# Optimization experiments

Measured on AMD Instinct MI355X. Metric: run time of the kernel, lower is better.

Reference implementation:

```python
import jax, jax.numpy as jnp
import numpy as np

SD = 4          # spixel_downsize
EPS = 1e-5      # BatchNorm eps
SLOPE = 0.01    # nn.LeakyReLU() default negative_slope


def deconv3d(x, w, stride, pad):
    # w is in torch ConvTranspose3d layout: (in_ch, out_ch, kd, kh, kw).
    # Transposed conv == conv with lhs_dilation=stride, flipped kernel,
    # padding (k-1-p) per spatial dim.
    kd, kh, kw = w.shape[2], w.shape[3], w.shape[4]
    wc = jnp.transpose(jnp.flip(w, axis=(2, 3, 4)), (1, 0, 2, 3, 4))  # OIDHW
    pads = [(kd - 1 - pad[0],) * 2, (kh - 1 - pad[1],) * 2, (kw - 1 - pad[2],) * 2]
    return jax.lax.conv_general_dilated(
        x, wc, window_strides=(1, 1, 1), padding=pads,
        lhs_dilation=(stride, stride, stride),
        dimension_numbers=('NCDHW', 'OIDHW', 'NCDHW'))


def bn_lrelu(x, g, b, relu=True):
    # inference BatchNorm3d with running_mean=0, running_var=1 (fresh BN)
    scale = (g / jnp.sqrt(1.0 + EPS)).reshape(1, -1, 1, 1, 1)
    y = x * scale + b.reshape(1, -1, 1, 1, 1)
    return jax.nn.leaky_relu(y, SLOPE) if relu else y


def _sl(s):
    # shift s in {+1, 0, -1} -> (agg slice, cost slice) along one spatial dim
    if s == 1:
        return slice(SD, None), slice(None, -SD)
    if s == 0:
        return slice(None), slice(None)
    return slice(None, -SD), slice(SD, None)


def setup_inputs() -> dict:
    key = jax.random.key(0)
    ks = jax.random.split(key, 8)
    b, d, h, w = 1, 24, 64, 128
    f32 = jnp.float32
    cv1 = jax.random.normal(ks[0], (b, 32, d, h, w), f32)                 # cv[-1]
    cv0 = jax.random.normal(ks[1], (b, 16, 2 * d, 2 * h, 2 * w), f32)     # cv[-2]
    sp = jax.random.uniform(ks[2], (b, 9, 4 * h, 4 * w), f32)             # superpixel probs
    w0a = jax.random.normal(ks[3], (32, 32, 3, 1, 1), f32) * 0.05
    w0b = jax.random.normal(ks[4], (32, 16, 4, 2, 2), f32) * 0.05
    w1a = jax.random.normal(ks[5], (32, 16, 3, 1, 1), f32) * 0.05
    w1b = jax.random.normal(ks[6], (16, 1, 4, 2, 2), f32) * 0.05
    g0, g1, g2, g3 = (jnp.ones((c,), f32) for c in (32, 16, 16, 1))
    b0, b1, b2, b3 = (jnp.zeros((c,), f32) for c in (32, 16, 16, 1))
    return dict(cv1=cv1, cv0=cv0, sp=sp, w0a=w0a, w0b=w0b, w1a=w1a, w1b=w1b,
                g0=g0, g1=g1, g2=g2, g3=g3, b0=b0, b1=b1, b2=b2, b3=b3)


def reference(cv1, cv0, sp, w0a, w0b, w1a, w1b, g0, g1, g2, g3, b0, b1, b2, b3):
    # conv[0]: BasicConv(32->32, k(3,1,1), s1, p(1,0,0)) + BasicConv(32->16, k(4,2,2), s2, p(1,0,0))
    x = bn_lrelu(deconv3d(cv1, w0a, 1, (1, 0, 0)), g0, b0)
    x = bn_lrelu(deconv3d(x, w0b, 2, (1, 0, 0)), g1, b1)
    x = jnp.concatenate((x, cv0), axis=1)
    # conv[1] (sp==2 branch): 32->16 then 16->out_dim, bn=relu=bnrelu=True
    x = bn_lrelu(deconv3d(x, w1a, 1, (1, 0, 0)), g2, b2)
    cost = bn_lrelu(deconv3d(x, w1b, 2, (1, 0, 0)), g3, b3)  # (b, 1, 4d, 4h, 4w)

    sp5 = sp[:, None]  # (b, 1, 9, H, W)
    agg = jnp.zeros_like(cost)
    k = 0
    for hy in (1, 0, -1):        # 9 fixed superpixel-neighbor shifts
        ah, ch = _sl(hy)
        for wx in (1, 0, -1):
            aw, cw = _sl(wx)
            wgt = sp5[:, :, k, ah, aw][:, :, None]  # (b,1,1,H',W')
            agg = agg.at[:, :, :, ah, aw].add(cost[:, :, :, ch, cw] * wgt)
            k += 1
    return agg
```

## Files before the change

### kernel.cpp

```cpp
#include <hip/hip_runtime.h>
#include <hip/hip_bf16.h>

typedef __hip_bfloat16 bf16;

constexpr int cD0 = 24,  cH0 = 64,  cW0 = 128;
constexpr int cD1 = 48,  cH1 = 128, cW1 = 256;
constexpr int cD2 = 96,  cH2 = 256, cW2 = 512;
constexpr size_t PL0 = (size_t)cD0 * cH0 * cW0;
constexpr size_t PL1 = (size_t)cD1 * cH1 * cW1;
constexpr size_t PL2 = (size_t)cD2 * cH2 * cW2;

__device__ __forceinline__ float b2f(bf16 v) { return __bfloat162float(v); }
__device__ __forceinline__ bf16  f2b(float v) { return __float2bfloat16(v); }
__device__ __forceinline__ float lrelu(float v) { return v >= 0.f ? v : 0.01f * v; }
__device__ __forceinline__ float us2f(ushort u) { return __uint_as_float(((uint)u) << 16); }
__device__ __forceinline__ ushort f2us(float v) { return __bfloat16_as_ushort(f2b(v)); }

__global__ __launch_bounds__(256) void kA(const float* __restrict__ cv1,
                                          const float* __restrict__ w0a,
                                          const float* __restrict__ g0,
                                          const float* __restrict__ b0,
                                          bf16* __restrict__ x1) {
    __shared__ float lw[3][32][32];
    __shared__ float lsc[32], lbi[32];
    const int tid = threadIdx.x;
    for (int i = tid; i < 32 * 32 * 3; i += 256) {
        int ci = i / 96, r = i - ci * 96, co = r / 3, u = r - co * 3;
        lw[u][ci][co] = w0a[i];
    }
    if (tid < 32) {
        lsc[tid] = g0[tid] * (1.0f / sqrtf(1.0f + 1e-5f));
        lbi[tid] = b0[tid];
    }
    __syncthreads();

    const int pos = blockIdx.x * 256 + tid;
    const int x = pos & (cW0 - 1);
    const int y = (pos >> 7) & (cH0 - 1);
    const int z = pos >> 13;

    float acc[32];
    #pragma unroll
    for (int co = 0; co < 32; ++co) acc[co] = 0.f;

    #pragma unroll
    for (int u = 0; u < 3; ++u) {
        const int zi = z + 1 - u;
        if (zi < 0 || zi >= cD0) continue;
        const float* src = cv1 + (size_t)(zi * cH0 + y) * cW0 + x;
        float v[32];
        #pragma unroll
        for (int ci = 0; ci < 32; ++ci) v[ci] = src[ci * PL0];
        #pragma unroll
        for (int ci = 0; ci < 32; ++ci) {
            const float4* wp = (const float4*)&lw[u][ci][0];
            #pragma unroll
            for (int q = 0; q < 8; ++q) {
                float4 wv = wp[q];
                acc[4*q+0] += v[ci] * wv.x; acc[4*q+1] += v[ci] * wv.y;
                acc[4*q+2] += v[ci] * wv.z; acc[4*q+3] += v[ci] * wv.w;
            }
        }
    }
    #pragma unroll
    for (int co = 0; co < 32; ++co)
        x1[co * PL0 + (size_t)(z * cH0 + y) * cW0 + x] =
            f2b(lrelu(acc[co] * lsc[co] + lbi[co]));
}

__global__ __launch_bounds__(256) void kB(const bf16* __restrict__ x1,
                                          const float* __restrict__ w0b,
                                          const float* __restrict__ g1,
                                          const float* __restrict__ b1,
                                          bf16* __restrict__ x2) {
    __shared__ float lw[4][2][32][2][16];
    __shared__ float lsc[16], lbi[16];
    const int tid = threadIdx.x;
    for (int i = tid; i < 8192; i += 256) {
        int ci = i >> 8, co = (i >> 4) & 15, kd = (i >> 2) & 3, kh = (i >> 1) & 1, kw = i & 1;
        lw[kd][kh][ci][kw][co] = w0b[i];
    }
    if (tid < 16) {
        lsc[tid] = g1[tid] * (1.0f / sqrtf(1.0f + 1e-5f));
        lbi[tid] = b1[tid];
    }
    __syncthreads();

    const int t    = blockIdx.x * 256 + tid;
    const int lane = t & 63;
    const int wv_  = (t >> 6) & 3;
    const int b_   = t >> 8;
    const int oh = b_ & 127;
    const int od = (b_ >> 7) * 4 + wv_;
    const int ih = oh >> 1, kh = oh & 1;
    const int p  = (od + 1) & 1;
    const int iw0 = 2 * lane;

    float acc[4][16];
    #pragma unroll
    for (int k = 0; k < 4; ++k)
        #pragma unroll
        for (int co = 0; co < 16; ++co) acc[k][co] = 0.f;

    #pragma unroll
    for (int j = 0; j < 2; ++j) {
        const int kd = p + 2 * j;
        const int id = (od + 1 - kd) >> 1;
        if (id < 0 || id >= cD0) continue;
        const bf16* src = x1 + (size_t)(id * cH0 + ih) * cW0 + iw0;
        uint px[32];
        #pragma unroll
        for (int ci = 0; ci < 32; ++ci)
            px[ci] = *(const uint*)(src + ci * PL0);
        #pragma unroll
        for (int ci = 0; ci < 32; ++ci) {
            const float v0 = us2f((ushort)(px[ci] & 0xffffu));
            const float v1 = us2f((ushort)(px[ci] >> 16));
            const float4* wp0 = (const float4*)&lw[kd][kh][ci][0][0];
            const float4* wp1 = (const float4*)&lw[kd][kh][ci][1][0];
            #pragma unroll
            for (int q = 0; q < 4; ++q) {
                float4 w0 = wp0[q], w1 = wp1[q];
                acc[0][4*q+0] += v0 * w0.x; acc[0][4*q+1] += v0 * w0.y;
                acc[0][4*q+2] += v0 * w0.z; acc[0][4*q+3] += v0 * w0.w;
                acc[1][4*q+0] += v0 * w1.x; acc[1][4*q+1] += v0 * w1.y;
                acc[1][4*q+2] += v0 * w1.z; acc[1][4*q+3] += v0 * w1.w;
                acc[2][4*q+0] += v1 * w0.x; acc[2][4*q+1] += v1 * w0.y;
                acc[2][4*q+2] += v1 * w0.z; acc[2][4*q+3] += v1 * w0.w;
                acc[3][4*q+0] += v1 * w1.x; acc[3][4*q+1] += v1 * w1.y;
                acc[3][4*q+2] += v1 * w1.z; acc[3][4*q+3] += v1 * w1.w;
            }
        }
    }
    const size_t obase = (size_t)(od * cH1 + oh) * cW1 + 4 * lane;
    #pragma unroll
    for (int co = 0; co < 16; ++co) {
        ushort4 s;
        s.x = f2us(lrelu(acc[0][co] * lsc[co] + lbi[co]));
        s.y = f2us(lrelu(acc[1][co] * lsc[co] + lbi[co]));
        s.z = f2us(lrelu(acc[2][co] * lsc[co] + lbi[co]));
        s.w = f2us(lrelu(acc[3][co] * lsc[co] + lbi[co]));
        *(ushort4*)(x2 + co * PL1 + obase) = s;
    }
}

__global__ __launch_bounds__(256) void kD(const bf16* __restrict__ x2,
                                          const float* __restrict__ cv0,
                                          const float* __restrict__ w1a,
                                          const float* __restrict__ g2,
                                          const float* __restrict__ b2v,
                                          bf16* __restrict__ x3) {
    __shared__ float lw[3][32][16];
    __shared__ float lsc[16], lbi[16];
    const int tid = threadIdx.x;
    for (int i = tid; i < 1536; i += 256) {
        int ci = i / 48, r = i - ci * 48, co = r / 3, u = r - co * 3;
        lw[u][ci][co] = w1a[i];
    }
    if (tid < 16) {
        lsc[tid] = g2[tid] * (1.0f / sqrtf(1.0f + 1e-5f));
        lbi[tid] = b2v[tid];
    }
    __syncthreads();

    const int bid = blockIdx.x;
    const int b_  = (bid & 7) * 384 + (bid >> 3);
    const int zq = b_ % 12;
    const int yh = b_ / 12;
    const int h  = yh & 1;
    const int y  = yh >> 1;
    const int lane = tid & 63;
    const int wv_  = tid >> 6;
    const int z  = zq * 4 + wv_;
    const int x0 = h * 128 + 2 * lane;

    float acc[2][16];
    #pragma unroll
    for (int k = 0; k < 2; ++k)
        #pragma unroll
        for (int co = 0; co < 16; ++co) acc[k][co] = 0.f;

    #pragma unroll
    for (int u = 0; u < 3; ++u) {
        const int zi = z + 1 - u;
        if (zi < 0 || zi >= cD1) continue;
        const size_t base = (size_t)(zi * cH1 + y) * cW1 + x0;
        uint   px[16];
        float2 pc[16];
        #pragma unroll
        for (int ci = 0; ci < 16; ++ci)
            px[ci] = *(const uint*)(x2 + ci * PL1 + base);
        #pragma unroll
        for (int ci = 0; ci < 16; ++ci)
            pc[ci] = *(const float2*)(cv0 + ci * PL1 + base);
        #pragma unroll
        for (int ci = 0; ci < 16; ++ci) {
            const float v0 = us2f((ushort)(px[ci] & 0xffffu));
            const float v1 = us2f((ushort)(px[ci] >> 16));
            const float4* wp = (const float4*)&lw[u][ci][0];
            #pragma unroll
            for (int q = 0; q < 4; ++q) {
                float4 wv = wp[q];
                acc[0][4*q+0] += v0 * wv.x; acc[0][4*q+1] += v0 * wv.y;
                acc[0][4*q+2] += v0 * wv.z; acc[0][4*q+3] += v0 * wv.w;
                acc[1][4*q+0] += v1 * wv.x; acc[1][4*q+1] += v1 * wv.y;
                acc[1][4*q+2] += v1 * wv.z; acc[1][4*q+3] += v1 * wv.w;
            }
        }
        #pragma unroll
        for (int ci = 0; ci < 16; ++ci) {
            const float v0 = pc[ci].x, v1 = pc[ci].y;
            const float4* wp = (const float4*)&lw[u][16 + ci][0];
            #pragma unroll
            for (int q = 0; q < 4; ++q) {
                float4 wv = wp[q];
                acc[0][4*q+0] += v0 * wv.x; acc[0][4*q+1] += v0 * wv.y;
                acc[0][4*q+2] += v0 * wv.z; acc[0][4*q+3] += v0 * wv.w;
                acc[1][4*q+0] += v1 * wv.x; acc[1][4*q+1] += v1 * wv.y;
                acc[1][4*q+2] += v1 * wv.z; acc[1][4*q+3] += v1 * wv.w;
            }
        }
    }
    const size_t obase = (size_t)(z * cH1 + y) * cW1 + x0;
    #pragma unroll
    for (int co = 0; co < 16; ++co) {
        union { uint u32; ushort s[2]; } pk;
        pk.s[0] = f2us(lrelu(acc[0][co] * lsc[co] + lbi[co]));
        pk.s[1] = f2us(lrelu(acc[1][co] * lsc[co] + lbi[co]));
        *(uint*)(x3 + co * PL1 + obase) = pk.u32;
    }
}

__global__ __launch_bounds__(256) void kE(const bf16* __restrict__ x3,
                                          const float* __restrict__ w1b,
                                          const float* __restrict__ g3,
                                          const float* __restrict__ b3v,
                                          bf16* __restrict__ cost) {
    __shared__ float lw[256];
    const int tid = threadIdx.x;
    lw[tid] = w1b[tid];
    __syncthreads();

    const int t    = blockIdx.x * 256 + tid;
    const int lane = t & 63;
    const int wv_  = (t >> 6) & 3;
    const int b_   = t >> 8;
    const int iwp = lane + 64 * (b_ & 1);
    const int ih  = (b_ >> 1) & 127;
    const int od  = (b_ >> 8) * 4 + wv_;
    const int p   = (od + 1) & 1;
    const int iw0 = 2 * iwp;

    float a[2][2][2] = {};
    #pragma unroll
    for (int j = 0; j < 2; ++j) {
        const int kd = p + 2 * j;
        const int id = (od + 1 - kd) >> 1;
        if (id < 0 || id >= cD1) continue;
        const size_t base = (size_t)(id * cH1 + ih) * cW1 + iw0;
        uint px[16];
        #pragma unroll
        for (int ci = 0; ci < 16; ++ci)
            px[ci] = *(const uint*)(x3 + ci * PL1 + base);
        #pragma unroll
        for (int ci = 0; ci < 16; ++ci) {
            const float v0 = us2f((ushort)(px[ci] & 0xffffu));
            const float v1 = us2f((ushort)(px[ci] >> 16));
            const float* w = &lw[ci * 16 + kd * 4];
            a[0][0][0] += v0 * w[0]; a[0][0][1] += v0 * w[1];
            a[0][1][0] += v0 * w[2]; a[0][1][1] += v0 * w[3];
            a[1][0][0] += v1 * w[0]; a[1][0][1] += v1 * w[1];
            a[1][1][0] += v1 * w[2]; a[1][1][1] += v1 * w[3];
        }
    }
    const float sc = g3[0] * (1.0f / sqrtf(1.0f + 1e-5f));
    const float bi = b3v[0];
    const size_t ob = (size_t)(od * cH2 + 2 * ih) * cW2 + 4 * iwp;
    ushort4 s;
    s.x = f2us(lrelu(a[0][0][0] * sc + bi));
    s.y = f2us(lrelu(a[0][0][1] * sc + bi));
    s.z = f2us(lrelu(a[1][0][0] * sc + bi));
    s.w = f2us(lrelu(a[1][0][1] * sc + bi));
    *(ushort4*)(cost + ob) = s;
    s.x = f2us(lrelu(a[0][1][0] * sc + bi));
    s.y = f2us(lrelu(a[0][1][1] * sc + bi));
    s.z = f2us(lrelu(a[1][1][0] * sc + bi));
    s.w = f2us(lrelu(a[1][1][1] * sc + bi));
    *(ushort4*)(cost + ob + cW2) = s;
}

__global__ __launch_bounds__(256) void kF(const bf16* __restrict__ cost,
                                          const float* __restrict__ sp,
                                          float* __restrict__ out) {
    const int t    = blockIdx.x * 256 + threadIdx.x;
    const int lane = t & 63;
    const int rowq = t >> 6;
    const int x0 = 4 * (lane + 64 * (rowq & 1));
    const int y  = (rowq >> 1) & 255;
    const int d0 = (rowq >> 9) * 4;
    const size_t plane = (size_t)cH2 * cW2;

    float4 wq[9];
    int cyc[3], cxc[3];
    #pragma unroll
    for (int r = 0; r < 3; ++r) {
        const int cy = y - 4 * (1 - r);
        const bool vy = (cy >= 0) && (cy < cH2);
        cyc[r] = vy ? cy : 0;
        #pragma unroll
        for (int c = 0; c < 3; ++c) {
            const int cx = x0 - 4 * (1 - c);
            const bool vx = (cx >= 0) && (cx < cW2);
            if (r == 0) cxc[c] = vx ? cx : 0;
            if (vy && vx)
                wq[r*3+c] = *(const float4*)(sp + (size_t)(r*3+c) * plane + (size_t)y * cW2 + x0);
            else
                wq[r*3+c] = make_float4(0.f, 0.f, 0.f, 0.f);
        }
    }
    #pragma unroll
    for (int dd = 0; dd < 4; ++dd) {
        const int d = d0 + dd;
        const bf16* cp = cost + (size_t)d * plane;
        float ax = 0.f, ay = 0.f, az = 0.f, aw = 0.f;
        #pragma unroll
        for (int r = 0; r < 3; ++r) {
            const bf16* rp = cp + (size_t)cyc[r] * cW2;
            #pragma unroll
            for (int c = 0; c < 3; ++c) {
                const ushort4 u = *(const ushort4*)(rp + cxc[c]);
                const float4 w = wq[r*3+c];
                ax += w.x * us2f(u.x); ay += w.y * us2f(u.y);
                az += w.z * us2f(u.z); aw += w.w * us2f(u.w);
            }
        }
        float4 o; o.x = ax; o.y = ay; o.z = az; o.w = aw;
        *(float4*)(out + (size_t)d * plane + (size_t)y * cW2 + x0) = o;
    }
}

extern "C" void kernel_launch(void* const* d_in, const int* in_sizes, int n_in,
                              void* d_out, int out_size, void* d_ws, size_t ws_size,
                              hipStream_t stream) {
    const float* cv1 = (const float*)d_in[0];
    const float* cv0 = (const float*)d_in[1];
    const float* sp  = (const float*)d_in[2];
    const float* w0a = (const float*)d_in[3];
    const float* w0b = (const float*)d_in[4];
    const float* w1a = (const float*)d_in[5];
    const float* w1b = (const float*)d_in[6];
    const float* g0  = (const float*)d_in[7];
    const float* g1  = (const float*)d_in[8];
    const float* g2  = (const float*)d_in[9];
    const float* g3  = (const float*)d_in[10];
    const float* b0  = (const float*)d_in[11];
    const float* b1  = (const float*)d_in[12];
    const float* b2  = (const float*)d_in[13];
    const float* b3  = (const float*)d_in[14];

    char* ws = (char*)d_ws;
    bf16* x1   = (bf16*)(ws);
    bf16* x2   = (bf16*)(ws + 12582912);
    bf16* x3   = (bf16*)(ws + 62914560);
    bf16* cost = (bf16*)(ws);

    kA<<<768,  256, 0, stream>>>(cv1, w0a, g0, b0, x1);
    kB<<<1536, 256, 0, stream>>>(x1, w0b, g1, b1, x2);
    kD<<<3072, 256, 0, stream>>>(x2, cv0, w1a, g2, b2, x3);
    kE<<<6144, 256, 0, stream>>>(x3, w1b, g3, b3, cost);
    kF<<<3072, 256, 0, stream>>>(cost, sp, (float*)d_out);
}
```

Baseline: 411.1 us.

## Pre-transpose weights once and read them as uniform scalar loads

Adds a one-block kernel that rearranges all conv weights into a layout matched to each kernel, writing them into scratch at the tail of the output buffer. The conv kernels then read weights directly from global memory with wave-uniform indexing, which allows scalar loads, instead of staging them in LDS behind a barrier. kD now computes four output pixels per thread with half as many blocks, reusing each weight across more pixels. The cost is extra register pressure in kD and a dependency on the scratch area in d_out staying untouched until kF overwrites it.

```diff
diff --git a/kernel.cpp b/kernel.cpp
--- a/kernel.cpp
+++ b/kernel.cpp
@@ -16,32 +16,45 @@
 __device__ __forceinline__ float us2f(ushort u) { return __uint_as_float(((uint)u) << 16); }
 __device__ __forceinline__ ushort f2us(float v) { return __bfloat16_as_ushort(f2b(v)); }
 
+__global__ __launch_bounds__(256) void kW(const float* __restrict__ w0a,
+                                          const float* __restrict__ w0b,
+                                          const float* __restrict__ w1a,
+                                          const float* __restrict__ w1b,
+                                          float* __restrict__ wA,
+                                          float* __restrict__ wB,
+                                          float* __restrict__ wD,
+                                          float* __restrict__ wE) {
+    const int tid = threadIdx.x;
+    for (int i = tid; i < 3072; i += 256) {
+        int ci = i / 96, r = i - ci * 96, co = r / 3, u = r - co * 3;
+        wA[(u * 32 + ci) * 32 + co] = w0a[i];
+    }
+    for (int i = tid; i < 8192; i += 256) {
+        int ci = i >> 8, co = (i >> 4) & 15, kd = (i >> 2) & 3, kh = (i >> 1) & 1, kw = i & 1;
+        wB[(((kd * 2 + kh) * 32 + ci) * 2 + kw) * 16 + co] = w0b[i];
+    }
+    for (int i = tid; i < 1536; i += 256) {
+        int ci = i / 48, r = i - ci * 48, co = r / 3, u = r - co * 3;
+        wD[(u * 32 + ci) * 16 + co] = w1a[i];
+    }
+    {
+        int i = tid;
+        int ci = i >> 4, kd = (i >> 2) & 3, kh = (i >> 1) & 1, kw = i & 1;
+        wE[(kd * 4 + kh * 2 + kw) * 16 + ci] = w1b[i];
+    }
+}
+
 __global__ __launch_bounds__(256) void kA(const float* __restrict__ cv1,
-                                          const float* __restrict__ w0a,
+                                          const float* __restrict__ wA,
                                           const float* __restrict__ g0,
                                           const float* __restrict__ b0,
                                           bf16* __restrict__ x1) {
-    __shared__ float lw[3][32][32];
-    __shared__ float lsc[32], lbi[32];
-    const int tid = threadIdx.x;
-    for (int i = tid; i < 32 * 32 * 3; i += 256) {
-        int ci = i / 96, r = i - ci * 96, co = r / 3, u = r - co * 3;
-        lw[u][ci][co] = w0a[i];
-    }
-    if (tid < 32) {
-        lsc[tid] = g0[tid] * (1.0f / sqrtf(1.0f + 1e-5f));
-        lbi[tid] = b0[tid];
-    }
-    __syncthreads();
-
-    const int pos = blockIdx.x * 256 + tid;
+    const int pos = blockIdx.x * 256 + threadIdx.x;
     const int x = pos & (cW0 - 1);
     const int y = (pos >> 7) & (cH0 - 1);
     const int z = pos >> 13;
 
-    float acc[32];
-    #pragma unroll
-    for (int co = 0; co < 32; ++co) acc[co] = 0.f;
+    float acc[32] = {};
 
     #pragma unroll
     for (int u = 0; u < 3; ++u) {
@@ -53,54 +66,34 @@
         for (int ci = 0; ci < 32; ++ci) v[ci] = src[ci * PL0];
         #pragma unroll
         for (int ci = 0; ci < 32; ++ci) {
-            const float4* wp = (const float4*)&lw[u][ci][0];
-            #pragma unroll
-            for (int q = 0; q < 8; ++q) {
-                float4 wv = wp[q];
-                acc[4*q+0] += v[ci] * wv.x; acc[4*q+1] += v[ci] * wv.y;
-                acc[4*q+2] += v[ci] * wv.z; acc[4*q+3] += v[ci] * wv.w;
-            }
-        }
-    }
-    #pragma unroll
-    for (int co = 0; co < 32; ++co)
-        x1[co * PL0 + (size_t)(z * cH0 + y) * cW0 + x] =
-            f2b(lrelu(acc[co] * lsc[co] + lbi[co]));
+            const float* w = wA + (u * 32 + ci) * 32;
+            #pragma unroll
+            for (int q = 0; q < 32; ++q) acc[q] += v[ci] * w[q];
+        }
+    }
+    #pragma unroll
+    for (int co = 0; co < 32; ++co) {
+        const float sc = g0[co] * (1.0f / sqrtf(1.0f + 1e-5f));
+        const float bi = b0[co];
+        x1[co * PL0 + (size_t)(z * cH0 + y) * cW0 + x] = f2b(lrelu(acc[co] * sc + bi));
+    }
 }
 
 __global__ __launch_bounds__(256) void kB(const bf16* __restrict__ x1,
-                                          const float* __restrict__ w0b,
+                                          const float* __restrict__ wB,
                                           const float* __restrict__ g1,
                                           const float* __restrict__ b1,
                                           bf16* __restrict__ x2) {
-    __shared__ float lw[4][2][32][2][16];
-    __shared__ float lsc[16], lbi[16];
-    const int tid = threadIdx.x;
-    for (int i = tid; i < 8192; i += 256) {
-        int ci = i >> 8, co = (i >> 4) & 15, kd = (i >> 2) & 3, kh = (i >> 1) & 1, kw = i & 1;
-        lw[kd][kh][ci][kw][co] = w0b[i];
-    }
-    if (tid < 16) {
-        lsc[tid] = g1[tid] * (1.0f / sqrtf(1.0f + 1e-5f));
-        lbi[tid] = b1[tid];
-    }
-    __syncthreads();
-
-    const int t    = blockIdx.x * 256 + tid;
-    const int lane = t & 63;
-    const int wv_  = (t >> 6) & 3;
-    const int b_   = t >> 8;
+    const int lane = threadIdx.x & 63;
+    const int wv   = __builtin_amdgcn_readfirstlane(threadIdx.x >> 6);
+    const int b_   = blockIdx.x;
     const int oh = b_ & 127;
-    const int od = (b_ >> 7) * 4 + wv_;
+    const int od = (b_ >> 7) * 4 + wv;
     const int ih = oh >> 1, kh = oh & 1;
     const int p  = (od + 1) & 1;
     const int iw0 = 2 * lane;
 
-    float acc[4][16];
-    #pragma unroll
-    for (int k = 0; k < 4; ++k)
-        #pragma unroll
-        for (int co = 0; co < 16; ++co) acc[k][co] = 0.f;
+    float acc[4][16] = {};
 
     #pragma unroll
     for (int j = 0; j < 2; ++j) {
@@ -110,144 +103,115 @@
         const bf16* src = x1 + (size_t)(id * cH0 + ih) * cW0 + iw0;
         uint px[32];
         #pragma unroll
-        for (int ci = 0; ci < 32; ++ci)
-            px[ci] = *(const uint*)(src + ci * PL0);
+        for (int ci = 0; ci < 32; ++ci) px[ci] = *(const uint*)(src + ci * PL0);
+        const float* wkd = wB + (size_t)((kd * 2 + kh) * 32) * 32;
         #pragma unroll
         for (int ci = 0; ci < 32; ++ci) {
             const float v0 = us2f((ushort)(px[ci] & 0xffffu));
             const float v1 = us2f((ushort)(px[ci] >> 16));
-            const float4* wp0 = (const float4*)&lw[kd][kh][ci][0][0];
-            const float4* wp1 = (const float4*)&lw[kd][kh][ci][1][0];
-            #pragma unroll
-            for (int q = 0; q < 4; ++q) {
-                float4 w0 = wp0[q], w1 = wp1[q];
-                acc[0][4*q+0] += v0 * w0.x; acc[0][4*q+1] += v0 * w0.y;
-                acc[0][4*q+2] += v0 * w0.z; acc[0][4*q+3] += v0 * w0.w;
-                acc[1][4*q+0] += v0 * w1.x; acc[1][4*q+1] += v0 * w1.y;
-                acc[1][4*q+2] += v0 * w1.z; acc[1][4*q+3] += v0 * w1.w;
-                acc[2][4*q+0] += v1 * w0.x; acc[2][4*q+1] += v1 * w0.y;
-                acc[2][4*q+2] += v1 * w0.z; acc[2][4*q+3] += v1 * w0.w;
-                acc[3][4*q+0] += v1 * w1.x; acc[3][4*q+1] += v1 * w1.y;
-                acc[3][4*q+2] += v1 * w1.z; acc[3][4*q+3] += v1 * w1.w;
+            const float* w0 = wkd + ci * 32;
+            const float* w1 = w0 + 16;
+            #pragma unroll
+            for (int q = 0; q < 16; ++q) {
+                acc[0][q] += v0 * w0[q];
+                acc[1][q] += v0 * w1[q];
+                acc[2][q] += v1 * w0[q];
+                acc[3][q] += v1 * w1[q];
             }
         }
     }
     const size_t obase = (size_t)(od * cH1 + oh) * cW1 + 4 * lane;
     #pragma unroll
     for (int co = 0; co < 16; ++co) {
+        const float sc = g1[co] * (1.0f / sqrtf(1.0f + 1e-5f));
+        const float bi = b1[co];
         ushort4 s;
-        s.x = f2us(lrelu(acc[0][co] * lsc[co] + lbi[co]));
-        s.y = f2us(lrelu(acc[1][co] * lsc[co] + lbi[co]));
-        s.z = f2us(lrelu(acc[2][co] * lsc[co] + lbi[co]));
-        s.w = f2us(lrelu(acc[3][co] * lsc[co] + lbi[co]));
+        s.x = f2us(lrelu(acc[0][co] * sc + bi));
+        s.y = f2us(lrelu(acc[1][co] * sc + bi));
+        s.z = f2us(lrelu(acc[2][co] * sc + bi));
+        s.w = f2us(lrelu(acc[3][co] * sc + bi));
         *(ushort4*)(x2 + co * PL1 + obase) = s;
     }
 }
 
 __global__ __launch_bounds__(256) void kD(const bf16* __restrict__ x2,
                                           const float* __restrict__ cv0,
-                                          const float* __restrict__ w1a,
+                                          const float* __restrict__ wD,
                                           const float* __restrict__ g2,
                                           const float* __restrict__ b2v,
                                           bf16* __restrict__ x3) {
-    __shared__ float lw[3][32][16];
-    __shared__ float lsc[16], lbi[16];
-    const int tid = threadIdx.x;
-    for (int i = tid; i < 1536; i += 256) {
-        int ci = i / 48, r = i - ci * 48, co = r / 3, u = r - co * 3;
-        lw[u][ci][co] = w1a[i];
-    }
-    if (tid < 16) {
-        lsc[tid] = g2[tid] * (1.0f / sqrtf(1.0f + 1e-5f));
-        lbi[tid] = b2v[tid];
-    }
-    __syncthreads();
-
     const int bid = blockIdx.x;
-    const int b_  = (bid & 7) * 384 + (bid >> 3);
+    const int b_  = (bid & 7) * 192 + (bid >> 3);
     const int zq = b_ % 12;
-    const int yh = b_ / 12;
-    const int h  = yh & 1;
-    const int y  = yh >> 1;
-    const int lane = tid & 63;
-    const int wv_  = tid >> 6;
-    const int z  = zq * 4 + wv_;
-    const int x0 = h * 128 + 2 * lane;
-
-    float acc[2][16];
-    #pragma unroll
-    for (int k = 0; k < 2; ++k)
-        #pragma unroll
-        for (int co = 0; co < 16; ++co) acc[k][co] = 0.f;
+    const int y  = b_ / 12;
+    const int lane = threadIdx.x & 63;
+    const int wv   = __builtin_amdgcn_readfirstlane(threadIdx.x >> 6);
+    const int z  = zq * 4 + wv;
+    const int x0 = 4 * lane;
+
+    float acc[4][16] = {};
 
     #pragma unroll
     for (int u = 0; u < 3; ++u) {
         const int zi = z + 1 - u;
         if (zi < 0 || zi >= cD1) continue;
         const size_t base = (size_t)(zi * cH1 + y) * cW1 + x0;
-        uint   px[16];
-        float2 pc[16];
-        #pragma unroll
-        for (int ci = 0; ci < 16; ++ci)
-            px[ci] = *(const uint*)(x2 + ci * PL1 + base);
-        #pragma unroll
-        for (int ci = 0; ci < 16; ++ci)
-            pc[ci] = *(const float2*)(cv0 + ci * PL1 + base);
-        #pragma unroll
-        for (int ci = 0; ci < 16; ++ci) {
-            const float v0 = us2f((ushort)(px[ci] & 0xffffu));
-            const float v1 = us2f((ushort)(px[ci] >> 16));
-            const float4* wp = (const float4*)&lw[u][ci][0];
-            #pragma unroll
-            for (int q = 0; q < 4; ++q) {
-                float4 wv = wp[q];
-                acc[0][4*q+0] += v0 * wv.x; acc[0][4*q+1] += v0 * wv.y;
-                acc[0][4*q+2] += v0 * wv.z; acc[0][4*q+3] += v0 * wv.w;
-                acc[1][4*q+0] += v1 * wv.x; acc[1][4*q+1] += v1 * wv.y;
-                acc[1][4*q+2] += v1 * wv.z; acc[1][4*q+3] += v1 * wv.w;
+        {
+            ushort4 px[16];
+            #pragma unroll
+            for (int ci = 0; ci < 16; ++ci) px[ci] = *(const ushort4*)(x2 + ci * PL1 + base);
+            #pragma unroll
+            for (int ci = 0; ci < 16; ++ci) {
+                const float v0 = us2f(px[ci].x), v1 = us2f(px[ci].y);
+                const float v2 = us2f(px[ci].z), v3 = us2f(px[ci].w);
+                const float* w = wD + (u * 32 + ci) * 16;
+                #pragma unroll
+                for (int q = 0; q < 16; ++q) {
+                    acc[0][q] += v0 * w[q]; acc[1][q] += v1 * w[q];
+                    acc[2][q] += v2 * w[q]; acc[3][q] += v3 * w[q];
+                }
             }
         }
-        #pragma unroll
-        for (int ci = 0; ci < 16; ++ci) {
-            const float v0 = pc[ci].x, v1 = pc[ci].y;
-            const float4* wp = (const float4*)&lw[u][16 + ci][0];
-            #pragma unroll
-            for (int q = 0; q < 4; ++q) {
-                float4 wv = wp[q];
-                acc[0][4*q+0] += v0 * wv.x; acc[0][4*q+1] += v0 * wv.y;
-                acc[0][4*q+2] += v0 * wv.z; acc[0][4*q+3] += v0 * wv.w;
-                acc[1][4*q+0] += v1 * wv.x; acc[1][4*q+1] += v1 * wv.y;
-                acc[1][4*q+2] += v1 * wv.z; acc[1][4*q+3] += v1 * wv.w;
+        {
+            float4 pc[16];
+            #pragma unroll
+            for (int ci = 0; ci < 16; ++ci) pc[ci] = *(const float4*)(cv0 + ci * PL1 + base);
+            #pragma unroll
+            for (int ci = 0; ci < 16; ++ci) {
+                const float* w = wD + (u * 32 + 16 + ci) * 16;
+                #pragma unroll
+                for (int q = 0; q < 16; ++q) {
+                    acc[0][q] += pc[ci].x * w[q]; acc[1][q] += pc[ci].y * w[q];
+                    acc[2][q] += pc[ci].z * w[q]; acc[3][q] += pc[ci].w * w[q];
+                }
             }
         }
     }
     const size_t obase = (size_t)(z * cH1 + y) * cW1 + x0;
     #pragma unroll
     for (int co = 0; co < 16; ++co) {
-        union { uint u32; ushort s[2]; } pk;
-        pk.s[0] = f2us(lrelu(acc[0][co] * lsc[co] + lbi[co]));
-        pk.s[1] = f2us(lrelu(acc[1][co] * lsc[co] + lbi[co]));
-        *(uint*)(x3 + co * PL1 + obase) = pk.u32;
+        const float sc = g2[co] * (1.0f / sqrtf(1.0f + 1e-5f));
+        const float bi = b2v[co];
+        ushort4 s;
+        s.x = f2us(lrelu(acc[0][co] * sc + bi));
+        s.y = f2us(lrelu(acc[1][co] * sc + bi));
+        s.z = f2us(lrelu(acc[2][co] * sc + bi));
+        s.w = f2us(lrelu(acc[3][co] * sc + bi));
+        *(ushort4*)(x3 + co * PL1 + obase) = s;
     }
 }
 
 __global__ __launch_bounds__(256) void kE(const bf16* __restrict__ x3,
-                                          const float* __restrict__ w1b,
+                                          const float* __restrict__ wE,
                                           const float* __restrict__ g3,
                                           const float* __restrict__ b3v,
                                           bf16* __restrict__ cost) {
-    __shared__ float lw[256];
-    const int tid = threadIdx.x;
-    lw[tid] = w1b[tid];
-    __syncthreads();
-
-    const int t    = blockIdx.x * 256 + tid;
-    const int lane = t & 63;
-    const int wv_  = (t >> 6) & 3;
-    const int b_   = t >> 8;
+    const int lane = threadIdx.x & 63;
+    const int wv   = __builtin_amdgcn_readfirstlane(threadIdx.x >> 6);
+    const int b_   = blockIdx.x;
     const int iwp = lane + 64 * (b_ & 1);
     const int ih  = (b_ >> 1) & 127;
-    const int od  = (b_ >> 8) * 4 + wv_;
+    const int od  = (b_ >> 8) * 4 + wv;
     const int p   = (od + 1) & 1;
     const int iw0 = 2 * iwp;
 
@@ -260,17 +224,16 @@
         const size_t base = (size_t)(id * cH1 + ih) * cW1 + iw0;
         uint px[16];
         #pragma unroll
-        for (int ci = 0; ci < 16; ++ci)
-            px[ci] = *(const uint*)(x3 + ci * PL1 + base);
+        for (int ci = 0; ci < 16; ++ci) px[ci] = *(const uint*)(x3 + ci * PL1 + base);
+        const float* w = wE + kd * 64;
         #pragma unroll
         for (int ci = 0; ci < 16; ++ci) {
             const float v0 = us2f((ushort)(px[ci] & 0xffffu));
             const float v1 = us2f((ushort)(px[ci] >> 16));
-            const float* w = &lw[ci * 16 + kd * 4];
-            a[0][0][0] += v0 * w[0]; a[0][0][1] += v0 * w[1];
-            a[0][1][0] += v0 * w[2]; a[0][1][1] += v0 * w[3];
-            a[1][0][0] += v1 * w[0]; a[1][0][1] += v1 * w[1];
-            a[1][1][0] += v1 * w[2]; a[1][1][1] += v1 * w[3];
+            a[0][0][0] += v0 * w[ci];      a[0][0][1] += v0 * w[16 + ci];
+            a[0][1][0] += v0 * w[32 + ci]; a[0][1][1] += v0 * w[48 + ci];
+            a[1][0][0] += v1 * w[ci];      a[1][0][1] += v1 * w[16 + ci];
+            a[1][1][0] += v1 * w[32 + ci]; a[1][1][1] += v1 * w[48 + ci];
         }
     }
     const float sc = g3[0] * (1.0f / sqrtf(1.0f + 1e-5f));
@@ -364,9 +327,16 @@
     bf16* x3   = (bf16*)(ws + 62914560);
     bf16* cost = (bf16*)(ws);
 
-    kA<<<768,  256, 0, stream>>>(cv1, w0a, g0, b0, x1);
-    kB<<<1536, 256, 0, stream>>>(x1, w0b, g1, b1, x2);
-    kD<<<3072, 256, 0, stream>>>(x2, cv0, w1a, g2, b2, x3);
-    kE<<<6144, 256, 0, stream>>>(x3, w1b, g3, b3, cost);
+    float* wbase = (float*)((char*)d_out + 50331648 - 65536);
+    float* wA = wbase;
+    float* wB = wbase + 3072;
+    float* wD = wbase + 3072 + 8192;
+    float* wE = wD + 1536;
+
+    kW<<<1,    256, 0, stream>>>(w0a, w0b, w1a, w1b, wA, wB, wD, wE);
+    kA<<<768,  256, 0, stream>>>(cv1, wA, g0, b0, x1);
+    kB<<<1536, 256, 0, stream>>>(x1, wB, g1, b1, x2);
+    kD<<<1536, 256, 0, stream>>>(x2, cv0, wD, g2, b2, x3);
+    kE<<<6144, 256, 0, stream>>>(x3, wE, g3, b3, cost);
     kF<<<3072, 256, 0, stream>>>(cost, sp, (float*)d_out);
 }
```

Result: slower. 439.4 us (+6.9%).
